# Kernel optimization log

Hardware: AMD Instinct MI355X
Metric: run time of the kernel (lower is better)

## Reference

```python
import jax, jax.numpy as jnp
import numpy as np

B, T, C, H = 2, 2048, 1024, 16
HD = C // H  # head dim = 64


def setup_inputs() -> dict:
    key = jax.random.key(0)
    k1, k2, k3 = jax.random.split(key, 3)
    scale_in = 1.0 / np.sqrt(C)
    x = jax.random.normal(k1, (B, T, C), dtype=jnp.float32)
    w_qkv = jax.random.normal(k2, (C, 3 * C), dtype=jnp.float32) * scale_in
    b_qkv = jnp.zeros((3 * C,), dtype=jnp.float32)
    w_out = jax.random.normal(k3, (C, C), dtype=jnp.float32) * scale_in
    b_out = jnp.zeros((C,), dtype=jnp.float32)
    return {"x": x, "w_qkv": w_qkv, "b_qkv": b_qkv, "w_out": w_out, "b_out": b_out}


def reference(x, w_qkv, b_qkv, w_out, b_out):
    Bq, Tq, Cq = x.shape
    qkv = x @ w_qkv + b_qkv                       # [B,T,3C]
    q, k, v = jnp.split(qkv, 3, axis=-1)          # each [B,T,C]
    # [B,T,C] -> [B,H,T,HD]
    q = q.reshape(Bq, Tq, H, HD).transpose(0, 2, 1, 3)
    k = k.reshape(Bq, Tq, H, HD).transpose(0, 2, 1, 3)
    v = v.reshape(Bq, Tq, H, HD).transpose(0, 2, 1, 3)
    scale = 1.0 / np.sqrt(HD)
    scores = jnp.einsum("bhqd,bhkd->bhqk", q, k) * scale  # [B,H,T,T]
    causal = jnp.tril(jnp.ones((Tq, Tq), dtype=bool))
    scores = jnp.where(causal[None, None], scores, jnp.finfo(scores.dtype).min)
    attn = jax.nn.softmax(scores, axis=-1)
    y = jnp.einsum("bhqk,bhkd->bhqd", attn, v)    # [B,H,T,HD]
    y = y.transpose(0, 2, 1, 3).reshape(Bq, Tq, Cq)
    return y @ w_out + b_out
```

## Files before the change

kernel.cpp:

```cpp
#include <hip/hip_runtime.h>
#include <hip/hip_bf16.h>


#define B_ 2
#define T_ 2048
#define C_ 1024
#define H_ 16
#define HD_ 64
#define M_ (B_ * T_)
#define N3_ (3 * C_)
#define QK2_ 2048
#define QSCALE 0.18033688f

typedef __attribute__((ext_vector_type(8))) short short8;
typedef __attribute__((ext_vector_type(4))) short short4v;
typedef __attribute__((ext_vector_type(4))) float floatx4;

__device__ __forceinline__ unsigned short f2b(float f) {
    __hip_bfloat16 h = __float2bfloat16(f);
    return *reinterpret_cast<unsigned short*>(&h);
}

__device__ __forceinline__ float fexp2(float x) {
#if __has_builtin(__builtin_amdgcn_exp2f)
    return __builtin_amdgcn_exp2f(x);
#else
    return exp2f(x);
#endif
}

__device__ __forceinline__ void glds16(const void* g, void* l) {
    __builtin_amdgcn_global_load_lds(
        (const __attribute__((address_space(1))) void*)g,
        (__attribute__((address_space(3))) void*)l, 16, 0, 0);
}

__global__ __launch_bounds__(256) void prep(
    const float* __restrict__ x, const float* __restrict__ w_qkv,
    const float* __restrict__ w_out, unsigned short* __restrict__ xb,
    unsigned short* __restrict__ wt1, unsigned short* __restrict__ wt2) {
    __shared__ float t[64][33];
    const int bi = blockIdx.x;
    const int tid = threadIdx.x;
    if (bi < 4096) {
        int i = (bi * 256 + tid) * 4;
        float4 v = *reinterpret_cast<const float4*>(x + i);
        short4v s;
        s[0] = (short)f2b(v.x); s[1] = (short)f2b(v.y);
        s[2] = (short)f2b(v.z); s[3] = (short)f2b(v.w);
        *reinterpret_cast<short4v*>(xb + i) = s;
        return;
    }
    const float* src; unsigned short* dst; int n0, k0, N;
    if (bi < 4096 + 1536) {
        int u = bi - 4096;
        src = w_qkv; dst = wt1; N = N3_;
        k0 = (u & 15) * 64; n0 = (u >> 4) * 32;
    } else {
        int u = bi - (4096 + 1536);
        src = w_out; dst = wt2; N = C_;
        k0 = (u & 15) * 64; n0 = (u >> 4) * 32;
    }
    const int tx = tid & 31, ty = tid >> 5;
#pragma unroll
    for (int i = 0; i < 8; i++)
        t[ty + i * 8][tx] = src[(size_t)(k0 + ty + i * 8) * N + n0 + tx];
    __syncthreads();
    const int row = tid >> 3;
    const int kp  = (tid & 7) * 8;
    short8 o;
#pragma unroll
    for (int j = 0; j < 8; j++) o[j] = (short)f2b(t[kp + j][row]);
    *reinterpret_cast<short8*>(&dst[(size_t)(n0 + row) * C_ + k0 + kp]) = o;
}

template<int EPI, int BN>
__global__ __launch_bounds__(256) void gemm_glds(
    const unsigned short* __restrict__ A, const unsigned short* __restrict__ Bt,
    const float* __restrict__ bias, void* __restrict__ Cp,
    unsigned short* __restrict__ vtp, int M, int N, int K) {
    constexpr int NI = BN / 32;
    __shared__ __align__(16) unsigned short Al[128 * 64];
    __shared__ __align__(16) unsigned short Bl[BN * 64];

    const int tid  = threadIdx.x;
    const int lane = tid & 63;
    const int w    = tid >> 6;
    const int c16  = lane & 15;
    const int quad = lane >> 4;
    const int NT  = N / BN;
    const int pe  = NT >> 3;
    const int xcd = blockIdx.x & 7;
    const int ii  = blockIdx.x >> 3;
    const int n0  = (xcd * pe + ii % pe) * BN;
    const int m0  = (ii / pe) * 128;
    const int wm = (w >> 1) * 64;
    const int wn = (w & 1) * (BN / 2);

    floatx4 acc[4][NI] = {};

    const int srow = lane >> 3;
    const int sch  = ((lane & 7) ^ srow) * 8;
    const unsigned short* ag = A + (size_t)(m0 + w * 32 + srow) * K + sch;
    const unsigned short* bg = Bt + (size_t)(n0 + w * (BN / 4) + srow) * K + sch;

    const int s7 = c16 & 7;

    for (int k0 = 0; k0 < K; k0 += 64) {
        __syncthreads();
#pragma unroll
        for (int i = 0; i < 4; i++)
            glds16(ag + k0 + (size_t)(i * 8) * K, &Al[(w * 32 + i * 8) * 64]);
#pragma unroll
        for (int i = 0; i < BN / 32; i++)
            glds16(bg + k0 + (size_t)(i * 8) * K,
                   &Bl[(w * (BN / 4) + i * 8) * 64]);
        __syncthreads();

        short8 af[4][2], bf[NI][2];
#pragma unroll
        for (int im = 0; im < 4; im++)
#pragma unroll
            for (int kk = 0; kk < 2; kk++)
                af[im][kk] = *reinterpret_cast<const short8*>(
                    &Al[(wm + im * 16 + c16) * 64 + ((kk * 4 + quad) ^ s7) * 8]);
#pragma unroll
        for (int in = 0; in < NI; in++)
#pragma unroll
            for (int kk = 0; kk < 2; kk++)
                bf[in][kk] = *reinterpret_cast<const short8*>(
                    &Bl[(wn + in * 16 + c16) * 64 + ((kk * 4 + quad) ^ s7) * 8]);
#pragma unroll
        for (int im = 0; im < 4; im++)
#pragma unroll
            for (int in = 0; in < NI; in++)
#pragma unroll
                for (int kk = 0; kk < 2; kk++)
                    acc[im][in] = __builtin_amdgcn_mfma_f32_16x16x32_bf16(
                        af[im][kk], bf[in][kk], acc[im][in], 0, 0, 0);
    }

    const int ncol = n0 + wn;
    float bv[NI];
#pragma unroll
    for (int in = 0; in < NI; in++) bv[in] = bias[ncol + in * 16 + c16];

    if (EPI == 0) {
        float* C = (float*)Cp;
#pragma unroll
        for (int im = 0; im < 4; im++)
#pragma unroll
            for (int r = 0; r < 4; r++) {
                int row = m0 + wm + im * 16 + quad * 4 + r;
#pragma unroll
                for (int in = 0; in < NI; in++)
                    C[(size_t)row * N + ncol + in * 16 + c16] =
                        acc[im][in][r] + bv[in];
            }
    } else {
        if (ncol < 2 * C_) {
            const float fac = (ncol < C_) ? QSCALE : 1.0f;
            unsigned short* qkp = (unsigned short*)Cp;
#pragma unroll
            for (int im = 0; im < 4; im++)
#pragma unroll
                for (int r = 0; r < 4; r++) {
                    int row = m0 + wm + im * 16 + quad * 4 + r;
#pragma unroll
                    for (int in = 0; in < NI; in++)
                        qkp[(size_t)row * QK2_ + ncol + in * 16 + c16] =
                            f2b((acc[im][in][r] + bv[in]) * fac);
                }
        } else {
#pragma unroll
            for (int im = 0; im < 4; im++) {
                int row0 = m0 + wm + im * 16 + quad * 4;
                int b  = row0 >> 11;
                int t0 = row0 & (T_ - 1);
#pragma unroll
                for (int in = 0; in < NI; in++) {
                    int dfull = ncol - 2 * C_ + in * 16 + c16;
                    short4v sv;
#pragma unroll
                    for (int r = 0; r < 4; r++)
                        sv[r] = (short)f2b(acc[im][in][r] + bv[in]);
                    *reinterpret_cast<short4v*>(
                        &vtp[(((size_t)(b << 10) + dfull) << 11) + t0]) = sv;
                }
            }
        }
    }
}

template<bool MASKED>
__device__ __forceinline__ void attn_tile2(
    const short8 af0[2], const short8 af1[2],
    const unsigned short* __restrict__ Kb,
    const unsigned short* __restrict__ Vb,
    unsigned short* __restrict__ pw,
    floatx4 O[2][4], float l[2],
    int row0, int kb, int c16, int quad) {
    const floatx4 z = {0.f, 0.f, 0.f, 0.f};
    const int sx  = c16 & 7;
    const int ch0 = (quad ^ sx) * 8;
    const int ch1 = ((quad + 4) ^ sx) * 8;
#pragma unroll
    for (int nt = 0; nt < 4; nt++) {
        const int rb = (nt * 16 + c16) * 64;
        short8 k0 = *reinterpret_cast<const short8*>(&Kb[rb + ch0]);
        short8 k1 = *reinterpret_cast<const short8*>(&Kb[rb + ch1]);
#pragma unroll
        for (int j = 0; j < 2; j++) {
            floatx4 t = __builtin_amdgcn_mfma_f32_16x16x32_bf16(k0, af0[j], z, 0, 0, 0);
            floatx4 s = __builtin_amdgcn_mfma_f32_16x16x32_bf16(k1, af1[j], t, 0, 0, 0);
            short4v p4;
#pragma unroll
            for (int r = 0; r < 4; r++) {
                float p;
                if (MASKED) {
                    int key = kb + nt * 16 + quad * 4 + r;
                    p = (key <= row0 + j * 16 + c16) ? fexp2(s[r]) : 0.f;
                } else {
                    p = fexp2(s[r]);
                }
                l[j] += p;
                p4[r] = (short)f2b(p);
            }
            const int pst = ((2 * nt + (quad >> 1)) ^ sx) * 8 + (quad & 1) * 4;
            *reinterpret_cast<short4v*>(&pw[j * 1024 + c16 * 64 + pst]) = p4;
        }
    }
    short8 pf0[2], pf1[2];
#pragma unroll
    for (int j = 0; j < 2; j++) {
        pf0[j] = *reinterpret_cast<const short8*>(&pw[j * 1024 + c16 * 64 + ch0]);
        pf1[j] = *reinterpret_cast<const short8*>(&pw[j * 1024 + c16 * 64 + ch1]);
    }
#pragma unroll
    for (int nt = 0; nt < 4; nt++) {
        const int rb = (nt * 16 + c16) * 64;
        short8 v0 = *reinterpret_cast<const short8*>(&Vb[rb + ch0]);
        short8 v1 = *reinterpret_cast<const short8*>(&Vb[rb + ch1]);
#pragma unroll
        for (int j = 0; j < 2; j++) {
            floatx4 t = __builtin_amdgcn_mfma_f32_16x16x32_bf16(pf0[j], v0, O[j][nt], 0, 0, 0);
            O[j][nt] = __builtin_amdgcn_mfma_f32_16x16x32_bf16(pf1[j], v1, t, 0, 0, 0);
        }
    }
}

__global__ __launch_bounds__(256, 4) void attn_mfma(
    const unsigned short* __restrict__ qk,
    const unsigned short* __restrict__ vt,
    unsigned short* __restrict__ y) {
    __shared__ __align__(16) unsigned short Kl[2][64 * 64];
    __shared__ __align__(16) unsigned short Vl[2][64 * 64];
    __shared__ __align__(16) unsigned short Pl[4 * 16 * 64];

    const int tid  = threadIdx.x;
    const int lane = tid & 63;
    const int w    = tid >> 6;
    const int wq   = w & 1;
    const int par  = w >> 1;
    const int c16  = lane & 15;
    const int quad = lane >> 4;
    const int bh = blockIdx.x & 31;
    const int t  = 31 - (blockIdx.x >> 5);
    const int b  = bh >> 4;
    const int h  = bh & 15;
    const int row0 = t * 64 + wq * 32;
    const int nch  = t + 1;

    const unsigned short* qrow = qk + (size_t)b * T_ * QK2_ + h * HD_;
    const unsigned short* krow = qrow + C_;
    const unsigned short* vrow = vt + ((size_t)bh << 6) * T_;

    short8 af0[2], af1[2];
#pragma unroll
    for (int j = 0; j < 2; j++) {
        af0[j] = *reinterpret_cast<const short8*>(
            qrow + (size_t)(row0 + j * 16 + c16) * QK2_ + quad * 8);
        af1[j] = *reinterpret_cast<const short8*>(
            qrow + (size_t)(row0 + j * 16 + c16) * QK2_ + 32 + quad * 8);
    }

    floatx4 O[2][4] = {};
    float l[2] = {0.f, 0.f};
    unsigned short* pw = &Pl[wq * 2048];

    const int r8 = lane >> 3;
    const int sw = ((lane & 7) ^ r8) * 8;

#pragma unroll
    for (int i = 0; i < 2; i++) {
        glds16(krow + (size_t)(w * 16 + i * 8 + r8) * QK2_ + sw,
               &Kl[0][(w * 16 + i * 8) * 64]);
        glds16(vrow + (size_t)(w * 16 + i * 8 + r8) * T_ + sw,
               &Vl[0][(w * 16 + i * 8) * 64]);
    }

    for (int c = 0; c < nch; c++) {
        __syncthreads();
        if (c + 1 < nch) {
            const int kb2 = (c + 1) * 64;
            const int nb = (c + 1) & 1;
#pragma unroll
            for (int i = 0; i < 2; i++) {
                glds16(krow + (size_t)(kb2 + w * 16 + i * 8 + r8) * QK2_ + sw,
                       &Kl[nb][(w * 16 + i * 8) * 64]);
                glds16(vrow + (size_t)(w * 16 + i * 8 + r8) * T_ + kb2 + sw,
                       &Vl[nb][(w * 16 + i * 8) * 64]);
            }
        }
        if ((c & 1) == par) {
            const int kb = c * 64;
            if (c + 1 < nch)
                attn_tile2<false>(af0, af1, Kl[c & 1], Vl[c & 1], pw, O, l,
                                  row0, kb, c16, quad);
            else
                attn_tile2<true>(af0, af1, Kl[c & 1], Vl[c & 1], pw, O, l,
                                 row0, kb, c16, quad);
        }
    }

    __syncthreads();
    float* Kf = (float*)&Kl[0][0];
    float* Vf = (float*)&Vl[0][0];
    if (par) {
#pragma unroll
        for (int j = 0; j < 2; j++) {
#pragma unroll
            for (int nt = 0; nt < 4; nt++)
                *reinterpret_cast<floatx4*>(
                    &Kf[(wq * 2 + j) * 1024 + lane * 16 + nt * 4]) = O[j][nt];
            Vf[(wq * 2 + j) * 64 + lane] = l[j];
        }
    }
    __syncthreads();
    if (par == 0) {
#pragma unroll
        for (int j = 0; j < 2; j++) {
#pragma unroll
            for (int nt = 0; nt < 4; nt++)
                O[j][nt] += *reinterpret_cast<const floatx4*>(
                    &Kf[(wq * 2 + j) * 1024 + lane * 16 + nt * 4]);
            float lj = l[j] + Vf[(wq * 2 + j) * 64 + lane];

            lj += __shfl_xor(lj, 16);
            lj += __shfl_xor(lj, 32);
            float lr[4];
#pragma unroll
            for (int r = 0; r < 4; r++)
                lr[r] = __shfl(lj, quad * 4 + r);

#pragma unroll
            for (int nt = 0; nt < 4; nt++)
#pragma unroll
                for (int r = 0; r < 4; r++) {
                    float val = O[j][nt][r] / fmaxf(lr[r], 1e-30f);
                    y[((size_t)b * T_ + row0 + j * 16 + quad * 4 + r) * C_ +
                      h * HD_ + nt * 16 + c16] = f2b(val);
                }
        }
    }
}

extern "C" void kernel_launch(void* const* d_in, const int* in_sizes, int n_in,
                              void* d_out, int out_size, void* d_ws, size_t ws_size,
                              hipStream_t stream) {
    const float* x     = (const float*)d_in[0];
    const float* w_qkv = (const float*)d_in[1];
    const float* b_qkv = (const float*)d_in[2];
    const float* w_out = (const float*)d_in[3];
    const float* b_out = (const float*)d_in[4];
    float* out = (float*)d_out;

    unsigned short* qkb = (unsigned short*)d_ws;
    unsigned short* vtb = qkb + (size_t)M_ * QK2_;
    unsigned short* yb  = vtb + (size_t)B_ * H_ * HD_ * T_;
    unsigned short* wt1 = yb + (size_t)M_ * C_;
    unsigned short* wt2 = wt1 + (size_t)N3_ * C_;
    unsigned short* xb  = wt2 + (size_t)C_ * C_;

    prep<<<4096 + 1536 + 512, 256, 0, stream>>>(x, w_qkv, w_out, xb, wt1, wt2);

    gemm_glds<1, 128><<<(N3_ / 128) * (M_ / 128), 256, 0, stream>>>(
        xb, wt1, b_qkv, qkb, vtb, M_, N3_, C_);

    attn_mfma<<<B_ * H_ * 32, 256, 0, stream>>>(qkb, vtb, yb);

    gemm_glds<0, 64><<<(C_ / 64) * (M_ / 128), 256, 0, stream>>>(
        yb, wt2, b_out, out, nullptr, M_, C_, C_);
}
```

Measured before the change: 189.1 us.

## Split attention keys across waves and keep P in registers, removing LDS round-trip

Each wave now handles all 64 query rows for a 32-key slice of each chunk instead of 32 query rows for all 64 keys. This lets the S accumulator layout feed the PV MFMA directly as the A operand, removing the P store and reload through shared memory and its buffer. In exchange each wave keeps a 4x4 O accumulator set and four Q fragment pairs, which raises register pressure, so launch bounds drop to 3 blocks per SM. The final reduction becomes a three-phase all-to-all sum of partial O across the four waves, with more barriers.

```diff
diff --git a/kernel.cpp b/kernel.cpp
--- a/kernel.cpp
+++ b/kernel.cpp
@@ -193,74 +193,84 @@
 }
 
 template<bool MASKED>
-__device__ __forceinline__ void attn_tile2(
-    const short8 af0[2], const short8 af1[2],
+__device__ __forceinline__ void attn_chunk32(
+    const short8 af[4][2],
     const unsigned short* __restrict__ Kb,
     const unsigned short* __restrict__ Vb,
-    unsigned short* __restrict__ pw,
-    floatx4 O[2][4], float l[2],
-    int row0, int kb, int c16, int quad) {
+    floatx4 O[4][4], float lacc[4],
+    int q0, int kb, int s, int c16, int quad) {
     const floatx4 z = {0.f, 0.f, 0.f, 0.f};
-    const int sx  = c16 & 7;
-    const int ch0 = (quad ^ sx) * 8;
-    const int ch1 = ((quad + 4) ^ sx) * 8;
-#pragma unroll
-    for (int nt = 0; nt < 4; nt++) {
-        const int rb = (nt * 16 + c16) * 64;
-        short8 k0 = *reinterpret_cast<const short8*>(&Kb[rb + ch0]);
-        short8 k1 = *reinterpret_cast<const short8*>(&Kb[rb + ch1]);
-#pragma unroll
-        for (int j = 0; j < 2; j++) {
-            floatx4 t = __builtin_amdgcn_mfma_f32_16x16x32_bf16(k0, af0[j], z, 0, 0, 0);
-            floatx4 s = __builtin_amdgcn_mfma_f32_16x16x32_bf16(k1, af1[j], t, 0, 0, 0);
-            short4v p4;
+    const int sxr = c16 & 7;
+
+    floatx4 sv[4][2];
+#pragma unroll
+    for (int sub = 0; sub < 2; sub++) {
+        const int krow = (s * 32 + sub * 16 + c16) * 64;
+        short8 kf0 = *reinterpret_cast<const short8*>(
+            &Kb[krow + ((quad) ^ sxr) * 8]);
+        short8 kf1 = *reinterpret_cast<const short8*>(
+            &Kb[krow + ((4 + quad) ^ sxr) * 8]);
+#pragma unroll
+        for (int qt = 0; qt < 4; qt++) {
+            floatx4 t0 = __builtin_amdgcn_mfma_f32_16x16x32_bf16(
+                kf0, af[qt][0], z, 0, 0, 0);
+            sv[qt][sub] = __builtin_amdgcn_mfma_f32_16x16x32_bf16(
+                kf1, af[qt][1], t0, 0, 0, 0);
+        }
+    }
+
+    short8 vf[4];
+#pragma unroll
+    for (int dt = 0; dt < 4; dt++) {
+        const int vr = (dt * 16 + c16) * 64;
+        short4v v0 = *reinterpret_cast<const short4v*>(
+            &Vb[vr + (((s * 4 + (quad >> 1)) ^ sxr) << 3) + (quad & 1) * 4]);
+        short4v v1 = *reinterpret_cast<const short4v*>(
+            &Vb[vr + (((s * 4 + 2 + (quad >> 1)) ^ sxr) << 3) + (quad & 1) * 4]);
+        short8 v;
+        v[0] = v0[0]; v[1] = v0[1]; v[2] = v0[2]; v[3] = v0[3];
+        v[4] = v1[0]; v[5] = v1[1]; v[6] = v1[2]; v[7] = v1[3];
+        vf[dt] = v;
+    }
+
+#pragma unroll
+    for (int qt = 0; qt < 4; qt++) {
+        short8 pf;
+        float ll = 0.f;
+#pragma unroll
+        for (int sub = 0; sub < 2; sub++) {
 #pragma unroll
             for (int r = 0; r < 4; r++) {
                 float p;
                 if (MASKED) {
-                    int key = kb + nt * 16 + quad * 4 + r;
-                    p = (key <= row0 + j * 16 + c16) ? fexp2(s[r]) : 0.f;
+                    int key = kb + s * 32 + sub * 16 + quad * 4 + r;
+                    p = (key <= q0 + qt * 16 + c16) ? fexp2(sv[qt][sub][r]) : 0.f;
                 } else {
-                    p = fexp2(s[r]);
+                    p = fexp2(sv[qt][sub][r]);
                 }
-                l[j] += p;
-                p4[r] = (short)f2b(p);
+                ll += p;
+                pf[sub * 4 + r] = (short)f2b(p);
             }
-            const int pst = ((2 * nt + (quad >> 1)) ^ sx) * 8 + (quad & 1) * 4;
-            *reinterpret_cast<short4v*>(&pw[j * 1024 + c16 * 64 + pst]) = p4;
-        }
-    }
-    short8 pf0[2], pf1[2];
-#pragma unroll
-    for (int j = 0; j < 2; j++) {
-        pf0[j] = *reinterpret_cast<const short8*>(&pw[j * 1024 + c16 * 64 + ch0]);
-        pf1[j] = *reinterpret_cast<const short8*>(&pw[j * 1024 + c16 * 64 + ch1]);
-    }
-#pragma unroll
-    for (int nt = 0; nt < 4; nt++) {
-        const int rb = (nt * 16 + c16) * 64;
-        short8 v0 = *reinterpret_cast<const short8*>(&Vb[rb + ch0]);
-        short8 v1 = *reinterpret_cast<const short8*>(&Vb[rb + ch1]);
-#pragma unroll
-        for (int j = 0; j < 2; j++) {
-            floatx4 t = __builtin_amdgcn_mfma_f32_16x16x32_bf16(pf0[j], v0, O[j][nt], 0, 0, 0);
-            O[j][nt] = __builtin_amdgcn_mfma_f32_16x16x32_bf16(pf1[j], v1, t, 0, 0, 0);
-        }
-    }
-}
-
-__global__ __launch_bounds__(256, 4) void attn_mfma(
+        }
+        lacc[qt] += ll;
+#pragma unroll
+        for (int dt = 0; dt < 4; dt++)
+            O[qt][dt] = __builtin_amdgcn_mfma_f32_16x16x32_bf16(
+                pf, vf[dt], O[qt][dt], 0, 0, 0);
+    }
+}
+
+__global__ __launch_bounds__(256, 3) void attn_mfma(
     const unsigned short* __restrict__ qk,
     const unsigned short* __restrict__ vt,
     unsigned short* __restrict__ y) {
     __shared__ __align__(16) unsigned short Kl[2][64 * 64];
     __shared__ __align__(16) unsigned short Vl[2][64 * 64];
-    __shared__ __align__(16) unsigned short Pl[4 * 16 * 64];
 
     const int tid  = threadIdx.x;
     const int lane = tid & 63;
     const int w    = tid >> 6;
-    const int wq   = w & 1;
+    const int s    = w & 1;
     const int par  = w >> 1;
     const int c16  = lane & 15;
     const int quad = lane >> 4;
@@ -268,25 +278,23 @@
     const int t  = 31 - (blockIdx.x >> 5);
     const int b  = bh >> 4;
     const int h  = bh & 15;
-    const int row0 = t * 64 + wq * 32;
-    const int nch  = t + 1;
+    const int q0 = t * 64;
+    const int nch = t + 1;
 
     const unsigned short* qrow = qk + (size_t)b * T_ * QK2_ + h * HD_;
     const unsigned short* krow = qrow + C_;
     const unsigned short* vrow = vt + ((size_t)bh << 6) * T_;
 
-    short8 af0[2], af1[2];
-#pragma unroll
-    for (int j = 0; j < 2; j++) {
-        af0[j] = *reinterpret_cast<const short8*>(
-            qrow + (size_t)(row0 + j * 16 + c16) * QK2_ + quad * 8);
-        af1[j] = *reinterpret_cast<const short8*>(
-            qrow + (size_t)(row0 + j * 16 + c16) * QK2_ + 32 + quad * 8);
-    }
-
-    floatx4 O[2][4] = {};
-    float l[2] = {0.f, 0.f};
-    unsigned short* pw = &Pl[wq * 2048];
+    short8 af[4][2];
+#pragma unroll
+    for (int qt = 0; qt < 4; qt++)
+#pragma unroll
+        for (int hh = 0; hh < 2; hh++)
+            af[qt][hh] = *reinterpret_cast<const short8*>(
+                qrow + (size_t)(q0 + qt * 16 + c16) * QK2_ + hh * 32 + quad * 8);
+
+    floatx4 O[4][4] = {};
+    float lacc[4] = {0.f, 0.f, 0.f, 0.f};
 
     const int r8 = lane >> 3;
     const int sw = ((lane & 7) ^ r8) * 8;
@@ -315,54 +323,52 @@
         if ((c & 1) == par) {
             const int kb = c * 64;
             if (c + 1 < nch)
-                attn_tile2<false>(af0, af1, Kl[c & 1], Vl[c & 1], pw, O, l,
-                                  row0, kb, c16, quad);
+                attn_chunk32<false>(af, Kl[c & 1], Vl[c & 1], O, lacc,
+                                    q0, kb, s, c16, quad);
             else
-                attn_tile2<true>(af0, af1, Kl[c & 1], Vl[c & 1], pw, O, l,
-                                 row0, kb, c16, quad);
+                attn_chunk32<true>(af, Kl[c & 1], Vl[c & 1], O, lacc,
+                                   q0, kb, s, c16, quad);
         }
     }
 
     __syncthreads();
-    float* Kf = (float*)&Kl[0][0];
-    float* Vf = (float*)&Vl[0][0];
-    if (par) {
-#pragma unroll
-        for (int j = 0; j < 2; j++) {
-#pragma unroll
-            for (int nt = 0; nt < 4; nt++)
-                *reinterpret_cast<floatx4*>(
-                    &Kf[(wq * 2 + j) * 1024 + lane * 16 + nt * 4]) = O[j][nt];
-            Vf[(wq * 2 + j) * 64 + lane] = l[j];
-        }
-    }
-    __syncthreads();
-    if (par == 0) {
-#pragma unroll
-        for (int j = 0; j < 2; j++) {
-#pragma unroll
-            for (int nt = 0; nt < 4; nt++)
-                O[j][nt] += *reinterpret_cast<const floatx4*>(
-                    &Kf[(wq * 2 + j) * 1024 + lane * 16 + nt * 4]);
-            float lj = l[j] + Vf[(wq * 2 + j) * 64 + lane];
-
-            lj += __shfl_xor(lj, 16);
-            lj += __shfl_xor(lj, 32);
-            float lr[4];
-#pragma unroll
-            for (int r = 0; r < 4; r++)
-                lr[r] = __shfl(lj, quad * 4 + r);
-
-#pragma unroll
-            for (int nt = 0; nt < 4; nt++)
-#pragma unroll
-                for (int r = 0; r < 4; r++) {
-                    float val = O[j][nt][r] / fmaxf(lr[r], 1e-30f);
-                    y[((size_t)b * T_ + row0 + j * 16 + quad * 4 + r) * C_ +
-                      h * HD_ + nt * 16 + c16] = f2b(val);
-                }
-        }
-    }
+    float* Of = (float*)&Kl[0][0];
+    float* Lb = (float*)&Vl[0][0];
+#pragma unroll
+    for (int qt = 0; qt < 4; qt++)
+        Lb[qt * 256 + w * 64 + lane] = lacc[qt];
+#pragma unroll
+    for (int ph = 1; ph <= 3; ph++) {
+        const int dqt = (w + ph) & 3;
+#pragma unroll
+        for (int dt = 0; dt < 4; dt++)
+            *reinterpret_cast<floatx4*>(
+                &Of[dqt * 1024 + dt * 256 + lane * 4]) = O[dqt][dt];
+        __syncthreads();
+#pragma unroll
+        for (int dt = 0; dt < 4; dt++)
+            O[w][dt] += *reinterpret_cast<const floatx4*>(
+                &Of[w * 1024 + dt * 256 + lane * 4]);
+        __syncthreads();
+    }
+
+    float lj = Lb[w * 256 + lane] + Lb[w * 256 + 64 + lane] +
+               Lb[w * 256 + 128 + lane] + Lb[w * 256 + 192 + lane];
+    lj += __shfl_xor(lj, 16);
+    lj += __shfl_xor(lj, 32);
+    float lr[4];
+#pragma unroll
+    for (int r = 0; r < 4; r++)
+        lr[r] = __shfl(lj, quad * 4 + r);
+
+#pragma unroll
+    for (int dt = 0; dt < 4; dt++)
+#pragma unroll
+        for (int r = 0; r < 4; r++) {
+            float val = O[w][dt][r] / fmaxf(lr[r], 1e-30f);
+            y[((size_t)b * T_ + q0 + w * 16 + quad * 4 + r) * C_ +
+              h * HD_ + dt * 16 + c16] = f2b(val);
+        }
 }
 
 extern "C" void kernel_launch(void* const* d_in, const int* in_sizes, int n_in,
```

Result: slower. 352.3 us (+86.3%).
